# Optimization experiments

Hardware: AMD Instinct MI355X
Metric: run time of the kernel (lower is better)

## Reference

```python
import jax, jax.numpy as jnp
import numpy as np

B = 65536      # total rows = env_batch(8192) * n_slave(8)
DIN = 256      # input_shape
H = 64         # slave_hidden_dim
A = 32         # attention_dim
NACT = 14      # n_actions
NS = 8         # n_slave


def setup_inputs() -> dict:
    key = jax.random.key(0)
    ks = jax.random.split(key, 12)
    s = 0.05
    return {
        "obs": jax.random.normal(ks[0], (B, DIN), jnp.float32),
        "hidden_state": jax.random.normal(ks[1], (B, H), jnp.float32),
        "enc_W": jax.random.normal(ks[2], (DIN, H), jnp.float32) * s,
        "enc_b": jnp.zeros((H,), jnp.float32),
        "gru_Wih": jax.random.normal(ks[3], (3 * H, H), jnp.float32) * s,
        "gru_Whh": jax.random.normal(ks[4], (3 * H, H), jnp.float32) * s,
        "gru_bih": jnp.zeros((3 * H,), jnp.float32),
        "gru_bhh": jnp.zeros((3 * H,), jnp.float32),
        "qW": jax.random.normal(ks[5], (H, A), jnp.float32) * s,
        "kW": jax.random.normal(ks[6], (H, A), jnp.float32) * s,
        "vW": jax.random.normal(ks[7], (H, A), jnp.float32) * s,
        "vb": jnp.zeros((A,), jnp.float32),
        "decW": jax.random.normal(ks[8], (H + A, NACT), jnp.float32) * s,
        "decb": jnp.zeros((NACT,), jnp.float32),
        "n_slave": NS,
    }


def reference(obs, hidden_state, enc_W, enc_b, gru_Wih, gru_Whh, gru_bih, gru_bhh,
              qW, kW, vW, vb, decW, decb, n_slave):
    # encoding + ReLU
    x = jax.nn.relu(obs @ enc_W + enc_b)                      # [B, H]
    # torch GRUCell: r,z,n gate order in weight rows
    gx = x @ gru_Wih.T + gru_bih                              # [B, 3H]
    gh = hidden_state @ gru_Whh.T + gru_bhh                   # [B, 3H]
    xr, xz, xn = jnp.split(gx, 3, axis=-1)
    hr, hz, hn = jnp.split(gh, 3, axis=-1)
    r = jax.nn.sigmoid(xr + hr)
    z = jax.nn.sigmoid(xz + hz)
    n = jnp.tanh(xn + r * hn)
    h_out = (1.0 - z) * n + z * hidden_state                  # [B, H]

    Ad = qW.shape[-1]
    q = (h_out @ qW).reshape(-1, n_slave, Ad)                 # [b, n, A]
    k = (h_out @ kW).reshape(-1, n_slave, Ad)
    v = jax.nn.relu(h_out @ vW + vb).reshape(-1, n_slave, Ad)

    # exclude-self attention == diagonal-masked softmax attention
    scores = jnp.einsum('bia,bja->bij', q, k) / jnp.sqrt(jnp.float32(Ad))
    eye = jnp.eye(n_slave, dtype=bool)
    scores = jnp.where(eye, jnp.float32(-1e9), scores)
    attn = jax.nn.softmax(scores, axis=-1)                    # [b, n, n]
    xatt = jnp.einsum('bij,bja->bia', attn, v).reshape(-1, Ad)  # [B, A]

    out = jnp.concatenate([h_out, xatt], axis=-1) @ decW + decb  # [B, n_actions]
    return (out, h_out)
```

## Files before the change

kernel.cpp:

```cpp
#include <hip/hip_runtime.h>


#define NACT 14
#define BTOT 65536

typedef unsigned int  u32;
typedef unsigned short u16;
using short8 = __attribute__((ext_vector_type(8))) short;
using f32x4  = __attribute__((ext_vector_type(4))) float;

#define ENC0 0
#define WIH0 16384
#define WHH0 28672
#define QKV0 40960
#define DEC0 47104
#define WTOT 48640

#define DATA0 40960
#define WAVEU16 4608
#define BIASL 77824
#define LDSU16 78336

__device__ __align__(16) u16   g_wbuf[WTOT];
__device__ __align__(16) float g_bias[256];

__device__ __forceinline__ u32 f2bf_rne(float f){
  u32 x = __float_as_uint(f);
  return (x + 0x7fffu + ((x >> 16) & 1u)) >> 16;
}
__device__ __forceinline__ u32 pk2(float a, float b){
  u32 d;
  asm("v_cvt_pk_bf16_f32 %0, %1, %2" : "=v"(d) : "v"(a), "v"(b));
  return d;
}
__device__ __forceinline__ float blo(u32 u){ return __uint_as_float(u << 16); }
__device__ __forceinline__ float bhi(u32 u){ return __uint_as_float(u & 0xffff0000u); }
__device__ __forceinline__ float sigm(float x){ return 1.0f / (1.0f + __expf(-x)); }
__device__ __forceinline__ float tanhp(float x){ return 1.0f - 2.0f / (__expf(2.0f * x) + 1.0f); }
__device__ __forceinline__ short8 as_s8(uint4 v){ union { uint4 u; short8 s; } x; x.u = v; return x.s; }

#define MFMA16(a,b,c) __builtin_amdgcn_mfma_f32_16x16x32_bf16((a),(b),(c),0,0,0)

__global__ void prep(const float* __restrict__ encW, const float* __restrict__ Wih,
                     const float* __restrict__ Whh,  const float* __restrict__ qW,
                     const float* __restrict__ kW,   const float* __restrict__ vW,
                     const float* __restrict__ decW, const float* __restrict__ bih,
                     const float* __restrict__ bhh)
{
  int j = blockIdx.x * 256 + threadIdx.x;
  if (blockIdx.x == 0) {
    int n = threadIdx.x & 63, g = threadIdx.x >> 6;
    float v;
    if      (g == 0) v = bih[n]       + bhh[n];
    else if (g == 1) v = bih[64 + n]  + bhh[64 + n];
    else if (g == 2) v = bih[128 + n];
    else             v = bhh[128 + n];
    g_bias[threadIdx.x] = v;
  }
  if (j >= WTOT) return;
  int pos  = j & 511;
  int lane = pos >> 3, jj = pos & 7;
  int quad = lane >> 4, l16 = lane & 15;
  float val = 0.f;
  if (j < WIH0) {
    int f = j >> 9, ks = f >> 2, t = f & 3;
    int k = ks * 32 + quad * 8 + jj, n = 16 * t + l16;
    val = encW[k * 64 + n];
  } else if (j < WHH0) {
    int f = (j - WIH0) >> 9;
    int u = f / 6, g = (f >> 1) % 3, ks = f & 1;
    int wrow = 64 * g + 16 * u + l16, k = ks * 32 + quad * 8 + jj;
    val = Wih[wrow * 64 + k];
  } else if (j < QKV0) {
    int f = (j - WHH0) >> 9;
    int u = f / 6, g = (f >> 1) % 3, ks = f & 1;
    int wrow = 64 * g + 16 * u + l16, k = ks * 32 + quad * 8 + jj;
    val = Whh[wrow * 64 + k];
  } else if (j < DEC0) {
    int f = (j - QKV0) >> 9, t = f >> 1, ks = f & 1;
    int n = 16 * t + l16, mtx = n >> 5, nn = n & 31;
    int k = ks * 32 + quad * 8 + jj;
    val = (mtx == 0) ? qW[k * 32 + nn] * 0.17677669529663687f
        : (mtx == 1) ? kW[k * 32 + nn] : vW[k * 32 + nn];
  } else {
    int f = (j - DEC0) >> 9;
    int k = f * 32 + quad * 8 + jj, n = l16;
    if (n < 14) val = decW[k * 14 + n];
  }
  g_wbuf[j] = (u16)f2bf_rne(val);
}

struct Chunk {
  float4 ob[16];
  float4 hv[4];
};

__device__ __forceinline__ void issue_loads(int gr, const float* __restrict__ obs,
                                            const float* __restrict__ hid,
                                            int lane, int quad, int l16, Chunk& c)
{
  const float* ap = obs + (size_t)(gr + l16) * 256 + quad * 8;
  #pragma unroll
  for (int ks = 0; ks < 8; ks++) {
    c.ob[2 * ks]     = *(const float4*)(ap + ks * 32);
    c.ob[2 * ks + 1] = *(const float4*)(ap + ks * 32 + 4);
  }
  #pragma unroll
  for (int i = 0; i < 4; i++) {
    int cc = lane + 64 * i;
    c.hv[i] = ((const float4*)hid)[(size_t)(gr + (cc >> 4)) * 16 + (cc & 15)];
  }
}

template<bool LAST>
__device__ __forceinline__ void tile_body(
    int gr, int grN,
    u16* __restrict__ Xb, const u16* __restrict__ wl, const float* __restrict__ biasL,
    const float* __restrict__ obs, const float* __restrict__ hid,
    const float* __restrict__ encb, const float* __restrict__ vb,
    const float* __restrict__ decb, float* __restrict__ out,
    Chunk& cur, Chunk& nxt,
    int lane, int quad, int l16)
{
  u16*   Hb = Xb + 1152;
  float* Sf = (float*)(Xb + 2304);

  #pragma unroll
  for (int i = 0; i < 4; i++) {
    int c = lane + 64 * i;
    int lr = c >> 4, c4 = c & 15;
    *(uint2*)&Hb[lr * 72 + c4 * 4] =
        make_uint2(pk2(cur.hv[i].x, cur.hv[i].y), pk2(cur.hv[i].z, cur.hv[i].w));
  }

  f32x4 ce[4];
  #pragma unroll
  for (int t = 0; t < 4; t++) {
    float bv = encb[16 * t + l16];
    ce[t] = (f32x4){bv, bv, bv, bv};
  }
  #pragma unroll
  for (int ks = 0; ks < 8; ks++) {
    float4 a0 = cur.ob[2 * ks], a1 = cur.ob[2 * ks + 1];
    short8 a = as_s8(make_uint4(pk2(a0.x, a0.y), pk2(a0.z, a0.w), pk2(a1.x, a1.y), pk2(a1.z, a1.w)));
    #pragma unroll
    for (int t = 0; t < 4; t++) {
      short8 b = *(const short8*)&wl[ENC0 + (ks * 4 + t) * 512 + lane * 8];
      ce[t] = MFMA16(a, b, ce[t]);
    }
  }
  if (!LAST) issue_loads(grN, obs, hid, lane, quad, l16, nxt);
  #pragma unroll
  for (int t = 0; t < 4; t++)
    #pragma unroll
    for (int r = 0; r < 4; r++) {
      float xv = fmaxf(ce[t][r], 0.f);
      Xb[(quad * 4 + r) * 72 + 16 * t + l16] = (u16)pk2(xv, xv);
    }

  short8 ax[2], ah[2];
  #pragma unroll
  for (int ks = 0; ks < 2; ks++) {
    ax[ks] = *(const short8*)&Xb[l16 * 72 + ks * 32 + quad * 8];
    ah[ks] = *(const short8*)&Hb[l16 * 72 + ks * 32 + quad * 8];
  }
  #pragma unroll
  for (int u = 0; u < 4; u++) {
    f32x4 g6[6];
    #pragma unroll
    for (int t = 0; t < 6; t++) g6[t] = (f32x4){0.f, 0.f, 0.f, 0.f};
    #pragma unroll
    for (int g = 0; g < 3; g++) {
      #pragma unroll
      for (int ks = 0; ks < 2; ks++) {
        int f = (u * 3 + g) * 2 + ks;
        short8 bi = *(const short8*)&wl[WIH0 + f * 512 + lane * 8];
        short8 bh = *(const short8*)&wl[WHH0 + f * 512 + lane * 8];
        g6[g]     = MFMA16(ax[ks], bi, g6[g]);
        g6[3 + g] = MFMA16(ah[ks], bh, g6[3 + g]);
      }
    }
    int nc = 16 * u + l16;
    float brz = biasL[nc], bzz = biasL[64 + nc], bni = biasL[128 + nc], bnh = biasL[192 + nc];
    float hp[4];
    #pragma unroll
    for (int r = 0; r < 4; r++)
      hp[r] = blo(Hb[(quad * 4 + r) * 72 + nc]);
    #pragma unroll
    for (int r = 0; r < 4; r++) {
      float rg = sigm(g6[0][r] + g6[3][r] + brz);
      float zg = sigm(g6[1][r] + g6[4][r] + bzz);
      float nn = tanhp(g6[2][r] + bni + rg * (g6[5][r] + bnh));
      float ho = (1.f - zg) * nn + zg * hp[r];
      Hb[(quad * 4 + r) * 72 + nc] = (u16)pk2(ho, ho);
    }
  }

  short8 hx[2];
  #pragma unroll
  for (int ks = 0; ks < 2; ks++)
    hx[ks] = *(const short8*)&Hb[l16 * 72 + ks * 32 + quad * 8];
  f32x4 cq[6];
  #pragma unroll
  for (int t = 0; t < 6; t++) {
    float bv = (t >= 4) ? vb[16 * (t - 4) + l16] : 0.f;
    cq[t] = (f32x4){bv, bv, bv, bv};
  }
  #pragma unroll
  for (int ks = 0; ks < 2; ks++)
    #pragma unroll
    for (int t = 0; t < 6; t++) {
      short8 b = as_s8(*(const uint4*)&g_wbuf[QKV0 + (t * 2 + ks) * 512 + lane * 8]);
      cq[t] = MFMA16(hx[ks], b, cq[t]);
    }
  #pragma unroll
  for (int t = 0; t < 4; t++)
    #pragma unroll
    for (int r = 0; r < 4; r++)
      Sf[(quad * 4 + r) * 68 + 16 * t + l16] = cq[t][r];
  #pragma unroll
  for (int t = 4; t < 6; t++)
    #pragma unroll
    for (int r = 0; r < 4; r++)
      Xb[(quad * 4 + r) * 72 + 32 + 16 * (t - 4) + l16] =
          (u16)pk2(fmaxf(cq[t][r], 0.f), 0.f);

  {
    const int r_l = lane >> 2, s4 = lane & 3;
    const int gb = r_l & ~7, ri = r_l & 7;
    const float* fq = &Sf[r_l * 68];
    float sc[2];
    #pragma unroll
    for (int jj = 0; jj < 2; jj++) {
      int j = 2 * s4 + jj;
      const float* fk = &Sf[(gb + j) * 68 + 32];
      float d = 0.f;
      #pragma unroll
      for (int a4 = 0; a4 < 32; a4 += 4) {
        float4 q4 = *(const float4*)&fq[a4];
        float4 k4 = *(const float4*)&fk[a4];
        d += q4.x * k4.x + q4.y * k4.y + q4.z * k4.z + q4.w * k4.w;
      }
      sc[jj] = (j == ri) ? -1e30f : d;
    }
    float m = fmaxf(sc[0], sc[1]);
    m = fmaxf(m, __shfl_xor(m, 1));
    m = fmaxf(m, __shfl_xor(m, 2));
    float p[2], sum = 0.f;
    #pragma unroll
    for (int jj = 0; jj < 2; jj++) {
      int j = 2 * s4 + jj;
      p[jj] = (j == ri) ? 0.f : __expf(sc[jj] - m);
      sum += p[jj];
    }
    sum += __shfl_xor(sum, 1);
    sum += __shfl_xor(sum, 2);
    float inv = 1.f / sum;
    #pragma unroll
    for (int jj = 0; jj < 2; jj++)
      Sf[r_l * 68 + 2 * s4 + jj] = p[jj] * inv;
    float xa[8];
    #pragma unroll
    for (int u = 0; u < 8; u++) xa[u] = 0.f;
    #pragma unroll
    for (int j = 0; j < 8; j++) {
      float aj = Sf[r_l * 68 + j];
      const u16* vp = &Xb[(gb + j) * 72 + 32 + 8 * s4];
      uint4 v0 = *(const uint4*)vp;
      xa[0] += aj * blo(v0.x); xa[1] += aj * bhi(v0.x);
      xa[2] += aj * blo(v0.y); xa[3] += aj * bhi(v0.y);
      xa[4] += aj * blo(v0.z); xa[5] += aj * bhi(v0.z);
      xa[6] += aj * blo(v0.w); xa[7] += aj * bhi(v0.w);
    }
    u16* xp = &Xb[r_l * 72 + 8 * s4];
    *(uint4*)xp = make_uint4(pk2(xa[0], xa[1]), pk2(xa[2], xa[3]),
                             pk2(xa[4], xa[5]), pk2(xa[6], xa[7]));
  }

  {
    float db = (l16 < NACT) ? decb[l16] : 0.f;
    f32x4 co = (f32x4){db, db, db, db};
    #pragma unroll
    for (int ks = 0; ks < 2; ks++) {
      short8 b = as_s8(*(const uint4*)&g_wbuf[DEC0 + ks * 512 + lane * 8]);
      short8 a = *(const short8*)&Hb[l16 * 72 + ks * 32 + quad * 8];
      co = MFMA16(a, b, co);
    }
    short8 b2 = as_s8(*(const uint4*)&g_wbuf[DEC0 + 2 * 512 + lane * 8]);
    short8 a2 = *(const short8*)&Xb[l16 * 72 + quad * 8];
    co = MFMA16(a2, b2, co);
    if (l16 < NACT)
      #pragma unroll
      for (int r = 0; r < 4; r++)
        out[(size_t)(gr + quad * 4 + r) * NACT + l16] = co[r];
  }

  {
    float* outH = out + (size_t)BTOT * NACT;
    #pragma unroll
    for (int i = 0; i < 2; i++) {
      int c = lane + 64 * i, lr = c >> 3, j = c & 7;
      uint4 u = *(const uint4*)&Hb[lr * 72 + 8 * j];
      *(float4*)(outH + (size_t)(gr + lr) * 64 + 8 * j) =
          make_float4(blo(u.x), bhi(u.x), blo(u.y), bhi(u.y));
      *(float4*)(outH + (size_t)(gr + lr) * 64 + 8 * j + 4) =
          make_float4(blo(u.z), bhi(u.z), blo(u.w), bhi(u.w));
    }
  }
}

__global__ __launch_bounds__(512, 2)
void commslave_main(const float* __restrict__ obs,  const float* __restrict__ hid,
                    const float* __restrict__ encb, const float* __restrict__ vb,
                    const float* __restrict__ decb, float* __restrict__ out)
{
  __shared__ __align__(16) u16 lds[LDSU16];

  const int tid  = threadIdx.x;
  const int w    = tid >> 6;
  const int lane = tid & 63;
  const int quad = lane >> 4;
  const int l16  = lane & 15;

  const int gr0 = blockIdx.x * 256 + w * 16;
  const int gr1 = gr0 + 128;

  Chunk c0, c1;
  issue_loads(gr0, obs, hid, lane, quad, l16, c0);

  {
    uint4* dw = (uint4*)lds;
    const uint4* sw = (const uint4*)g_wbuf;
    #pragma unroll
    for (int i = 0; i < 10; i++)
      dw[tid + 512 * i] = sw[tid + 512 * i];
    if (tid < 64) ((uint4*)(lds + BIASL))[tid] = ((const uint4*)g_bias)[tid];
  }
  __syncthreads();

  u16* Xb = lds + DATA0 + w * WAVEU16;
  const float* biasL = (const float*)(lds + BIASL);

  tile_body<false>(gr0, gr1, Xb, lds, biasL, obs, hid, encb, vb, decb, out,
                   c0, c1, lane, quad, l16);
  tile_body<true >(gr1, 0,   Xb, lds, biasL, obs, hid, encb, vb, decb, out,
                   c1, c0, lane, quad, l16);
}

extern "C" void kernel_launch(void* const* d_in, const int* in_sizes, int n_in,
                              void* d_out, int out_size, void* d_ws, size_t ws_size,
                              hipStream_t stream) {
  (void)in_sizes; (void)n_in; (void)d_ws; (void)ws_size; (void)out_size;
  const float* obs  = (const float*)d_in[0];
  const float* hid  = (const float*)d_in[1];
  const float* encW = (const float*)d_in[2];
  const float* encb = (const float*)d_in[3];
  const float* Wih  = (const float*)d_in[4];
  const float* Whh  = (const float*)d_in[5];
  const float* bih  = (const float*)d_in[6];
  const float* bhh  = (const float*)d_in[7];
  const float* qW   = (const float*)d_in[8];
  const float* kW   = (const float*)d_in[9];
  const float* vW   = (const float*)d_in[10];
  const float* vb   = (const float*)d_in[11];
  const float* decW = (const float*)d_in[12];
  const float* decb = (const float*)d_in[13];
  float* out = (float*)d_out;

  prep<<<(WTOT + 255) / 256, 256, 0, stream>>>(encW, Wih, Whh, qW, kW, vW, decW, bih, bhh);
  commslave_main<<<256, 512, 0, stream>>>(obs, hid, encb, vb, decb, out);
}
```

Before: 145.9 us.

## Fuse weight prep into main kernel and keep QKV/decoder fragments in registers

Removes the separate prep kernel launch by having each block convert fp32 weights to bf16 and swizzle them directly into LDS. The QKV and decoder weight fragments are built per-lane into registers instead of being read from global memory inside the tile loop. This saves a launch and a global round-trip, but every block now repeats the conversion work and reads strided fp32 weights. The extra register-resident fragments raise register pressure under the 512x2 launch bound.

```diff
diff --git a/kernel.cpp b/kernel.cpp
--- a/kernel.cpp
+++ b/kernel.cpp
@@ -12,22 +12,11 @@
 #define ENC0 0
 #define WIH0 16384
 #define WHH0 28672
-#define QKV0 40960
-#define DEC0 47104
-#define WTOT 48640
-
 #define DATA0 40960
 #define WAVEU16 4608
 #define BIASL 77824
 #define LDSU16 78336
 
-__device__ __align__(16) u16   g_wbuf[WTOT];
-__device__ __align__(16) float g_bias[256];
-
-__device__ __forceinline__ u32 f2bf_rne(float f){
-  u32 x = __float_as_uint(f);
-  return (x + 0x7fffu + ((x >> 16) & 1u)) >> 16;
-}
 __device__ __forceinline__ u32 pk2(float a, float b){
   u32 d;
   asm("v_cvt_pk_bf16_f32 %0, %1, %2" : "=v"(d) : "v"(a), "v"(b));
@@ -41,55 +30,6 @@
 
 #define MFMA16(a,b,c) __builtin_amdgcn_mfma_f32_16x16x32_bf16((a),(b),(c),0,0,0)
 
-__global__ void prep(const float* __restrict__ encW, const float* __restrict__ Wih,
-                     const float* __restrict__ Whh,  const float* __restrict__ qW,
-                     const float* __restrict__ kW,   const float* __restrict__ vW,
-                     const float* __restrict__ decW, const float* __restrict__ bih,
-                     const float* __restrict__ bhh)
-{
-  int j = blockIdx.x * 256 + threadIdx.x;
-  if (blockIdx.x == 0) {
-    int n = threadIdx.x & 63, g = threadIdx.x >> 6;
-    float v;
-    if      (g == 0) v = bih[n]       + bhh[n];
-    else if (g == 1) v = bih[64 + n]  + bhh[64 + n];
-    else if (g == 2) v = bih[128 + n];
-    else             v = bhh[128 + n];
-    g_bias[threadIdx.x] = v;
-  }
-  if (j >= WTOT) return;
-  int pos  = j & 511;
-  int lane = pos >> 3, jj = pos & 7;
-  int quad = lane >> 4, l16 = lane & 15;
-  float val = 0.f;
-  if (j < WIH0) {
-    int f = j >> 9, ks = f >> 2, t = f & 3;
-    int k = ks * 32 + quad * 8 + jj, n = 16 * t + l16;
-    val = encW[k * 64 + n];
-  } else if (j < WHH0) {
-    int f = (j - WIH0) >> 9;
-    int u = f / 6, g = (f >> 1) % 3, ks = f & 1;
-    int wrow = 64 * g + 16 * u + l16, k = ks * 32 + quad * 8 + jj;
-    val = Wih[wrow * 64 + k];
-  } else if (j < QKV0) {
-    int f = (j - WHH0) >> 9;
-    int u = f / 6, g = (f >> 1) % 3, ks = f & 1;
-    int wrow = 64 * g + 16 * u + l16, k = ks * 32 + quad * 8 + jj;
-    val = Whh[wrow * 64 + k];
-  } else if (j < DEC0) {
-    int f = (j - QKV0) >> 9, t = f >> 1, ks = f & 1;
-    int n = 16 * t + l16, mtx = n >> 5, nn = n & 31;
-    int k = ks * 32 + quad * 8 + jj;
-    val = (mtx == 0) ? qW[k * 32 + nn] * 0.17677669529663687f
-        : (mtx == 1) ? kW[k * 32 + nn] : vW[k * 32 + nn];
-  } else {
-    int f = (j - DEC0) >> 9;
-    int k = f * 32 + quad * 8 + jj, n = l16;
-    if (n < 14) val = decW[k * 14 + n];
-  }
-  g_wbuf[j] = (u16)f2bf_rne(val);
-}
-
 struct Chunk {
   float4 ob[16];
   float4 hv[4];
@@ -116,6 +56,7 @@
 __device__ __forceinline__ void tile_body(
     int gr, int grN,
     u16* __restrict__ Xb, const u16* __restrict__ wl, const float* __restrict__ biasL,
+    const short8 (&qkvf)[12], const short8 (&decf)[3],
     const float* __restrict__ obs, const float* __restrict__ hid,
     const float* __restrict__ encb, const float* __restrict__ vb,
     const float* __restrict__ decb, float* __restrict__ out,
@@ -209,10 +150,8 @@
   #pragma unroll
   for (int ks = 0; ks < 2; ks++)
     #pragma unroll
-    for (int t = 0; t < 6; t++) {
-      short8 b = as_s8(*(const uint4*)&g_wbuf[QKV0 + (t * 2 + ks) * 512 + lane * 8]);
-      cq[t] = MFMA16(hx[ks], b, cq[t]);
-    }
+    for (int t = 0; t < 6; t++)
+      cq[t] = MFMA16(hx[ks], qkvf[t * 2 + ks], cq[t]);
   #pragma unroll
   for (int t = 0; t < 4; t++)
     #pragma unroll
@@ -282,13 +221,11 @@
     f32x4 co = (f32x4){db, db, db, db};
     #pragma unroll
     for (int ks = 0; ks < 2; ks++) {
-      short8 b = as_s8(*(const uint4*)&g_wbuf[DEC0 + ks * 512 + lane * 8]);
       short8 a = *(const short8*)&Hb[l16 * 72 + ks * 32 + quad * 8];
-      co = MFMA16(a, b, co);
-    }
-    short8 b2 = as_s8(*(const uint4*)&g_wbuf[DEC0 + 2 * 512 + lane * 8]);
+      co = MFMA16(a, decf[ks], co);
+    }
     short8 a2 = *(const short8*)&Xb[l16 * 72 + quad * 8];
-    co = MFMA16(a2, b2, co);
+    co = MFMA16(a2, decf[2], co);
     if (l16 < NACT)
       #pragma unroll
       for (int r = 0; r < 4; r++)
@@ -311,8 +248,13 @@
 
 __global__ __launch_bounds__(512, 2)
 void commslave_main(const float* __restrict__ obs,  const float* __restrict__ hid,
-                    const float* __restrict__ encb, const float* __restrict__ vb,
-                    const float* __restrict__ decb, float* __restrict__ out)
+                    const float* __restrict__ encW, const float* __restrict__ encb,
+                    const float* __restrict__ Wih,  const float* __restrict__ Whh,
+                    const float* __restrict__ bih,  const float* __restrict__ bhh,
+                    const float* __restrict__ qW,   const float* __restrict__ kW,
+                    const float* __restrict__ vW,   const float* __restrict__ vb,
+                    const float* __restrict__ decW, const float* __restrict__ decb,
+                    float* __restrict__ out)
 {
   __shared__ __align__(16) u16 lds[LDSU16];
 
@@ -328,23 +270,77 @@
   Chunk c0, c1;
   issue_loads(gr0, obs, hid, lane, quad, l16, c0);
 
-  {
-    uint4* dw = (uint4*)lds;
-    const uint4* sw = (const uint4*)g_wbuf;
-    #pragma unroll
-    for (int i = 0; i < 10; i++)
-      dw[tid + 512 * i] = sw[tid + 512 * i];
-    if (tid < 64) ((uint4*)(lds + BIASL))[tid] = ((const uint4*)g_bias)[tid];
+  short8 qkvf[12], decf[3];
+  #pragma unroll
+  for (int t = 0; t < 6; t++) {
+    const float* src = (t < 2) ? qW : (t < 4) ? kW : vW;
+    const int nn = 16 * (t & 1) + l16;
+    #pragma unroll
+    for (int ks = 0; ks < 2; ks++) {
+      float e[8];
+      #pragma unroll
+      for (int jj = 0; jj < 8; jj++)
+        e[jj] = src[(ks * 32 + quad * 8 + jj) * 32 + nn];
+      if (t < 2)
+        #pragma unroll
+        for (int jj = 0; jj < 8; jj++) e[jj] *= 0.17677669529663687f;
+      qkvf[t * 2 + ks] = as_s8(make_uint4(pk2(e[0], e[1]), pk2(e[2], e[3]),
+                                          pk2(e[4], e[5]), pk2(e[6], e[7])));
+    }
+  }
+  #pragma unroll
+  for (int ks = 0; ks < 3; ks++) {
+    float e[8];
+    #pragma unroll
+    for (int jj = 0; jj < 8; jj++)
+      e[jj] = (l16 < NACT) ? decW[(ks * 32 + quad * 8 + jj) * 14 + l16] : 0.f;
+    decf[ks] = as_s8(make_uint4(pk2(e[0], e[1]), pk2(e[2], e[3]),
+                                pk2(e[4], e[5]), pk2(e[6], e[7])));
+  }
+
+  #pragma unroll
+  for (int ii = 0; ii < 8; ii++) {
+    int fi = ii * 512 + tid;
+    float4 v = ((const float4*)encW)[fi];
+    int k = fi >> 4, n0 = (fi & 15) << 2;
+    int base = ENC0 + ((k >> 5) * 4 + (n0 >> 4)) * 512
+             + (((k >> 3) & 3) * 16 + (n0 & 15)) * 8 + (k & 7);
+    lds[base]      = (u16)pk2(v.x, v.x);
+    lds[base + 8]  = (u16)pk2(v.y, v.y);
+    lds[base + 16] = (u16)pk2(v.z, v.z);
+    lds[base + 24] = (u16)pk2(v.w, v.w);
+  }
+
+  #pragma unroll
+  for (int ii = 0; ii < 6; ii++) {
+    int fi = ii * 512 + tid;
+    float4 a = ((const float4*)Wih)[fi];
+    float4 b = ((const float4*)Whh)[fi];
+    int wrow = fi >> 4, k0 = (fi & 15) << 2;
+    int f = ((((wrow >> 4) & 3) * 3 + (wrow >> 6)) * 2 + (k0 >> 5)) * 512
+          + (((k0 >> 3) & 3) * 16 + (wrow & 15)) * 8 + (k0 & 7);
+    *(uint2*)&lds[WIH0 + f] = make_uint2(pk2(a.x, a.y), pk2(a.z, a.w));
+    *(uint2*)&lds[WHH0 + f] = make_uint2(pk2(b.x, b.y), pk2(b.z, b.w));
+  }
+
+  if (tid < 256) {
+    int n = tid & 63, g = tid >> 6;
+    float v;
+    if      (g == 0) v = bih[n]       + bhh[n];
+    else if (g == 1) v = bih[64 + n]  + bhh[64 + n];
+    else if (g == 2) v = bih[128 + n];
+    else             v = bhh[128 + n];
+    ((float*)(lds + BIASL))[tid] = v;
   }
   __syncthreads();
 
   u16* Xb = lds + DATA0 + w * WAVEU16;
   const float* biasL = (const float*)(lds + BIASL);
 
-  tile_body<false>(gr0, gr1, Xb, lds, biasL, obs, hid, encb, vb, decb, out,
-                   c0, c1, lane, quad, l16);
-  tile_body<true >(gr1, 0,   Xb, lds, biasL, obs, hid, encb, vb, decb, out,
-                   c1, c0, lane, quad, l16);
+  tile_body<false>(gr0, gr1, Xb, lds, biasL, qkvf, decf, obs, hid, encb, vb,
+                   decb, out, c0, c1, lane, quad, l16);
+  tile_body<true >(gr1, 0,   Xb, lds, biasL, qkvf, decf, obs, hid, encb, vb,
+                   decb, out, c1, c0, lane, quad, l16);
 }
 
 extern "C" void kernel_launch(void* const* d_in, const int* in_sizes, int n_in,
@@ -367,6 +363,6 @@
   const float* decb = (const float*)d_in[13];
   float* out = (float*)d_out;
 
-  prep<<<(WTOT + 255) / 256, 256, 0, stream>>>(encW, Wih, Whh, qW, kW, vW, decW, bih, bhh);
-  commslave_main<<<256, 512, 0, stream>>>(obs, hid, encb, vb, decb, out);
-}
+  commslave_main<<<256, 512, 0, stream>>>(obs, hid, encW, encb, Wih, Whh,
+                                          bih, bhh, qW, kW, vW, vb, decW, decb, out);
+}
```

New measurement: 145.3 us. Within noise of the previous version (-0.4%).
